# Kernel optimization log

Measured on AMD Instinct MI355X. Metric: run time of the kernel, lower is better.

## Reference

```python
import jax, jax.numpy as jnp
import numpy as np

N = 100000       # nodes
E = 1600000      # edges (before self loops)
F_IN = 128       # input features
H = 4            # heads
C1, C2 = 32, 16  # per-head channels of conv1/conv2


def setup_inputs() -> dict:
    key = jax.random.key(0)
    ks = jax.random.split(key, 12)
    x = jax.random.normal(ks[0], (N, F_IN), jnp.float32)
    edge_index = jax.random.randint(ks[1], (2, E), 0, N, dtype=jnp.int32)
    s1 = 1.0 / np.sqrt(F_IN)
    s2 = 1.0 / np.sqrt(H * C1)
    return {
        "x": x,
        "edge_index": edge_index,
        "W1": jax.random.normal(ks[2], (F_IN, H * C1), jnp.float32) * s1,
        "a_src1": jax.random.normal(ks[3], (1, H, C1), jnp.float32) * s1,
        "a_dst1": jax.random.normal(ks[4], (1, H, C1), jnp.float32) * s1,
        "b1": jnp.zeros((H * C1,), jnp.float32),
        "W2": jax.random.normal(ks[5], (H * C1, H * C2), jnp.float32) * s2,
        "a_src2": jax.random.normal(ks[6], (1, H, C2), jnp.float32) * s2,
        "a_dst2": jax.random.normal(ks[7], (1, H, C2), jnp.float32) * s2,
        "b2": jnp.zeros((H * C2,), jnp.float32),
        "fc_w": jax.random.normal(ks[8], (H * C2, 2), jnp.float32) * (1.0 / np.sqrt(H * C2)),
        "fc_b": jnp.zeros((2,), jnp.float32),
    }


def gat_layer(x, edge_index, W, a_src, a_dst, b, heads, ch):
    """PyG GATConv: concat=True, negative_slope=0.2 (self loops already in edge_index)."""
    n = x.shape[0]
    h = (x @ W).reshape(n, heads, ch)                      # [N,H,C]
    alpha_src = jnp.sum(h * a_src, axis=-1)                # [N,H]
    alpha_dst = jnp.sum(h * a_dst, axis=-1)                # [N,H]
    src, dst = edge_index[0], edge_index[1]                # edge j->i: src=j, dst=i
    e = jax.nn.leaky_relu(alpha_src[src] + alpha_dst[dst], 0.2)  # [E,H]
    # scatter-softmax over incoming edges of each destination node
    m = jax.ops.segment_max(e, dst, num_segments=n)
    m = jnp.where(jnp.isfinite(m), m, 0.0)
    ex = jnp.exp(e - m[dst])
    s = jax.ops.segment_sum(ex, dst, num_segments=n)
    alpha = ex / s[dst]                                    # self loops guarantee s > 0
    out = jax.ops.segment_sum(alpha[:, :, None] * h[src], dst, num_segments=n)
    return out.reshape(n, heads * ch) + b


def reference(x, edge_index, W1, a_src1, a_dst1, b1, W2, a_src2, a_dst2, b2, fc_w, fc_b):
    n = x.shape[0]
    loops = jnp.arange(n, dtype=edge_index.dtype)
    ei = jnp.concatenate([edge_index, jnp.stack([loops, loops])], axis=1)  # add self loops once
    h = jax.nn.relu(gat_layer(x, ei, W1, a_src1, a_dst1, b1, H, C1))
    h = gat_layer(h, ei, W2, a_src2, a_dst2, b2, H, C2)
    g = jnp.sum(h, axis=0, keepdims=True)  # global_add_pool, batch = all zeros -> single graph
    return g @ fc_w + fc_b
```

## Files before the change

kernel.cpp:

```cpp
#include <hip/hip_runtime.h>
#include <hip/hip_bf16.h>
#include <math.h>


using pkh2 = decltype(__builtin_amdgcn_cvt_pkrtz(0.f, 0.f));
typedef __fp16 half8v __attribute__((ext_vector_type(8)));
typedef __attribute__((ext_vector_type(4))) float f32x4;

__device__ __forceinline__ unsigned cvt2h(float a, float b) {
    pkh2 r = __builtin_amdgcn_cvt_pkrtz(a, b);
    return __builtin_bit_cast(unsigned, r);
}
__device__ __forceinline__ unsigned short f2h(float f) {
    return __builtin_bit_cast(unsigned short, (_Float16)f);
}

__device__ __forceinline__ float fdot2b(unsigned wp, unsigned hp, float c) {
#if __has_builtin(__builtin_amdgcn_fdot2)
    return __builtin_amdgcn_fdot2(__builtin_bit_cast(pkh2, wp),
                                  __builtin_bit_cast(pkh2, hp), c, false);
#else
    pkh2 w = __builtin_bit_cast(pkh2, wp), h = __builtin_bit_cast(pkh2, hp);
    return fmaf((float)w[0], (float)h[0], fmaf((float)w[1], (float)h[1], c));
#endif
}


#define BCAP_LOG 13

__global__ __launch_bounds__(256) void bin_scatter_k(const int* __restrict__ ei,
                                                     int* __restrict__ bucketFill,
                                                     int2* __restrict__ binned,
                                                     int E, int N) {
    __shared__ int cnt[512];
    __shared__ int base[512];
    const int ITEMS = E + N;
    const int t = threadIdx.x;
    const int chunk0 = blockIdx.x * 4096;
    for (int b = t; b < 512; b += 256) cnt[b] = 0;
    __syncthreads();
    int s[16], d[16], r[16];
#pragma unroll
    for (int j = 0; j < 16; j++) {
        int i = chunk0 + j * 256 + t;
        if (i < ITEMS) {
            if (i < E) { s[j] = ei[i]; d[j] = ei[E + i]; }
            else       { s[j] = d[j] = i - E; }
            r[j] = atomicAdd(&cnt[d[j] >> 8], 1);
        } else d[j] = -1;
    }
    __syncthreads();
    for (int b = t; b < 512; b += 256) {
        int c = cnt[b];
        base[b] = c ? atomicAdd(&bucketFill[b], c) : 0;
    }
    __syncthreads();
#pragma unroll
    for (int j = 0; j < 16; j++)
        if (d[j] >= 0) {
            int b = d[j] >> 8;
            binned[((size_t)b << BCAP_LOG) + base[b] + r[j]] = make_int2(s[j], d[j]);
        }
}

__global__ void bucket_scan_k(const int* __restrict__ bucketCnt,
                              int* __restrict__ bucketOff, int NB) {
    __shared__ int ls[512];
    int t = threadIdx.x;
    int v = (t < NB) ? bucketCnt[t] : 0;
    ls[t] = v;
    __syncthreads();
    for (int off = 1; off < 512; off <<= 1) {
        int a = (t >= off) ? ls[t - off] : 0;
        __syncthreads();
        ls[t] += a;
        __syncthreads();
    }
    if (t < NB) bucketOff[t] = ls[t] - v;
}

__global__ void csr_build_k(const int2* __restrict__ binned,
                            const int* __restrict__ bucketOff,
                            const int* __restrict__ bucketCnt,
                            int* __restrict__ offs, int* __restrict__ csr,
                            int N, int ITEMS) {
    __shared__ int cnt[256];
    __shared__ int obase[256];
    __shared__ int fill[256];
    const int b = blockIdx.x, t = threadIdx.x;
    cnt[t] = 0; fill[t] = 0;
    __syncthreads();
    const int c = bucketCnt[b];
    const int2* bp = &binned[(size_t)b << BCAP_LOG];
    for (int i = t; i < c; i += 256)
        atomicAdd(&cnt[bp[i].y & 255], 1);
    __syncthreads();
    int v = cnt[t];
    obase[t] = v;
    __syncthreads();
    for (int off = 1; off < 256; off <<= 1) {
        int a = (t >= off) ? obase[t - off] : 0;
        __syncthreads();
        obase[t] += a;
        __syncthreads();
    }
    obase[t] -= v;
    const int beg = bucketOff[b];
    int node = b * 256 + t;
    if (node < N) offs[node] = beg + obase[t];
    if (node == N - 1) offs[N] = ITEMS;
    __syncthreads();
    for (int i = t; i < c; i += 256) {
        int2 sd = bp[i];
        int r = atomicAdd(&fill[sd.y & 255], 1);
        csr[beg + obase[sd.y & 255] + r] = sd.x;
    }
}


template<int NCOL, bool XF16>
__global__ __launch_bounds__(256) void gemm_alpha_mfma(
        const void* __restrict__ Xv, const float* __restrict__ W,
        const float* __restrict__ asrc, const float* __restrict__ adst,
        unsigned short* __restrict__ Y, float* __restrict__ As,
        float* __restrict__ Ad, int M) {
    constexpr int NT = NCOL / 16;
    __shared__ alignas(16) short alds[4 * 4 * 64 * 8];
    __shared__ alignas(16) short blds[NT * 4 * 64 * 8];

    const int t    = threadIdx.x;
    const int w    = t >> 6, lane = t & 63;
    const int row0 = blockIdx.x * 64;

    if constexpr (!XF16) {
        const float* X = (const float*)Xv;
#pragma unroll
        for (int i = 0; i < 8; i++) {
            int flat = (i * 256 + t) * 4;
            int r = flat >> 7, k0 = flat & 127;
            int gr = row0 + r;
            float4 v = make_float4(0.f, 0.f, 0.f, 0.f);
            if (gr < M) v = *(const float4*)&X[(size_t)gr * 128 + k0];
            uint2 u = make_uint2(cvt2h(v.x, v.y), cvt2h(v.z, v.w));
            int frag = ((r >> 4) * 4 + (k0 >> 5)) * 64 + ((((k0 & 31) >> 3) << 4) | (r & 15));
            *(uint2*)&alds[frag * 8 + (k0 & 7)] = u;
        }
    } else {
        const unsigned short* X = (const unsigned short*)Xv;
#pragma unroll
        for (int i = 0; i < 4; i++) {
            int flat = (i * 256 + t) * 8;
            int r = flat >> 7, k0 = flat & 127;
            int gr = row0 + r;
            uint4 v = make_uint4(0u, 0u, 0u, 0u);
            if (gr < M) v = *(const uint4*)&X[(size_t)gr * 128 + k0];
            int frag = ((r >> 4) * 4 + (k0 >> 5)) * 64 + ((((k0 & 31) >> 3) << 4) | (r & 15));
            *(uint4*)&alds[frag * 8] = v;
        }
    }

    {
        constexpr int KQ = 256 / NCOL;
        constexpr int BITER = 32 / KQ;
        int c = t % NCOL, kq = t / NCOL;
        int nt = c >> 4, n = c & 15;
#pragma unroll
        for (int i = 0; i < BITER; i++) {
            int k0 = (i * KQ + kq) * 4;
            uint2 u = make_uint2(
                cvt2h(W[(size_t)(k0 + 0) * NCOL + c], W[(size_t)(k0 + 1) * NCOL + c]),
                cvt2h(W[(size_t)(k0 + 2) * NCOL + c], W[(size_t)(k0 + 3) * NCOL + c]));
            int frag = (nt * 4 + (k0 >> 5)) * 64 + ((((k0 & 31) >> 3) << 4) | n);
            *(uint2*)&blds[frag * 8 + (k0 & 7)] = u;
        }
    }
    __syncthreads();

    f32x4 acc[NT];
#pragma unroll
    for (int nt = 0; nt < NT; nt++) acc[nt] = (f32x4){0.f, 0.f, 0.f, 0.f};
#pragma unroll
    for (int ks = 0; ks < 4; ks++) {
        half8v a = *(half8v*)&alds[((w * 4 + ks) * 64 + lane) * 8];
#pragma unroll
        for (int nt = 0; nt < NT; nt++) {
            half8v b = *(half8v*)&blds[((nt * 4 + ks) * 64 + lane) * 8];
            acc[nt] = __builtin_amdgcn_mfma_f32_16x16x32_f16(a, b, acc[nt], 0, 0, 0);
        }
    }

    const int g = lane >> 4, col = lane & 15;
    float ps[4][4] = {}, pd[4][4] = {};
#pragma unroll
    for (int nt = 0; nt < NT; nt++) {
        float av = asrc[nt * 16 + col];
        float dv = adst[nt * 16 + col];
        int h = (NCOL == 128) ? (nt >> 1) : nt;
#pragma unroll
        for (int j = 0; j < 4; j++) {
            float v = acc[nt][j];
            ps[j][h] = fmaf(v, av, ps[j][h]);
            pd[j][h] = fmaf(v, dv, pd[j][h]);
            int gr = row0 + w * 16 + 4 * g + j;
            if (gr < M) Y[(size_t)gr * NCOL + nt * 16 + col] = f2h(v);
        }
    }
#pragma unroll
    for (int m = 1; m < 16; m <<= 1) {
#pragma unroll
        for (int j = 0; j < 4; j++)
#pragma unroll
            for (int h = 0; h < 4; h++) {
                ps[j][h] += __shfl_xor(ps[j][h], m);
                pd[j][h] += __shfl_xor(pd[j][h], m);
            }
    }
    if (col == 0) {
#pragma unroll
        for (int j = 0; j < 4; j++) {
            int gr = row0 + w * 16 + 4 * g + j;
            if (gr < M) {
#pragma unroll
                for (int h = 0; h < 4; h++) {
                    As[gr * 4 + h] = ps[j][h];
                    Ad[gr * 4 + h] = pd[j][h];
                }
            }
        }
    }
}


template<bool RELU>
__global__ void agg128_k(const unsigned short* __restrict__ Hb,
                         const float* __restrict__ As, const float* __restrict__ Ad,
                         const int* __restrict__ offs, const int* __restrict__ csr,
                         const float* __restrict__ bias,
                         unsigned short* __restrict__ Outb, int n) {
    int wid  = (blockIdx.x * blockDim.x + threadIdx.x) >> 6;
    int lane = threadIdx.x & 63;
    if (wid >= n) return;
    const int g = lane >> 4;
    const int q = lane & 15;
    const int head = q >> 2;
    const int beg = offs[wid], end = offs[wid + 1];
    const float ad = Ad[wid * 4 + head];
    float acc[8];
#pragma unroll
    for (int k = 0; k < 8; k++) acc[k] = 0.f;
    float sw = 0.f;

    for (int cb = beg; cb < end; cb += 64) {
        const int nc = min(64, end - cb);
        const int sreg = csr[cb + (lane < nc ? lane : 0)];
        const int ncr = (nc + 15) & ~15;
        for (int j = 0; j < ncr; j += 16) {
            const int e0 = j + g, e1 = e0 + 4, e2 = e0 + 8, e3 = e0 + 12;
            const bool v0 = e0 < nc, v1 = e1 < nc, v2 = e2 < nc, v3 = e3 < nc;
            const int s0 = __shfl(sreg, v0 ? e0 : 0);
            const int s1 = __shfl(sreg, v1 ? e1 : 0);
            const int s2 = __shfl(sreg, v2 ? e2 : 0);
            const int s3 = __shfl(sreg, v3 ? e3 : 0);
            const uint4 hA = *(const uint4*)&Hb[(size_t)s0 * 128 + q * 8];
            const uint4 hB = *(const uint4*)&Hb[(size_t)s1 * 128 + q * 8];
            const uint4 hC = *(const uint4*)&Hb[(size_t)s2 * 128 + q * 8];
            const uint4 hD = *(const uint4*)&Hb[(size_t)s3 * 128 + q * 8];
            float ev0 = As[s0 * 4 + head] + ad; ev0 = ev0 > 0.f ? ev0 : 0.2f * ev0;
            float ev1 = As[s1 * 4 + head] + ad; ev1 = ev1 > 0.f ? ev1 : 0.2f * ev1;
            float ev2 = As[s2 * 4 + head] + ad; ev2 = ev2 > 0.f ? ev2 : 0.2f * ev2;
            float ev3 = As[s3 * 4 + head] + ad; ev3 = ev3 > 0.f ? ev3 : 0.2f * ev3;
            const float w0 = v0 ? __expf(ev0) : 0.f;
            const float w1 = v1 ? __expf(ev1) : 0.f;
            const float w2 = v2 ? __expf(ev2) : 0.f;
            const float w3 = v3 ? __expf(ev3) : 0.f;
            sw += (w0 + w1) + (w2 + w3);
            const unsigned wp01 = cvt2h(w0, w1);
            const unsigned wp23 = cvt2h(w2, w3);
#pragma unroll
            for (int k = 0; k < 4; k++) {
                unsigned a0 = (&hA.x)[k], a1 = (&hB.x)[k];
                unsigned a2 = (&hC.x)[k], a3 = (&hD.x)[k];
                acc[2 * k]     = fdot2b(wp01, __builtin_amdgcn_perm(a1, a0, 0x05040100u), acc[2 * k]);
                acc[2 * k]     = fdot2b(wp23, __builtin_amdgcn_perm(a3, a2, 0x05040100u), acc[2 * k]);
                acc[2 * k + 1] = fdot2b(wp01, __builtin_amdgcn_perm(a1, a0, 0x07060302u), acc[2 * k + 1]);
                acc[2 * k + 1] = fdot2b(wp23, __builtin_amdgcn_perm(a3, a2, 0x07060302u), acc[2 * k + 1]);
            }
        }
    }

    sw += __shfl_xor(sw, 16); sw += __shfl_xor(sw, 32);
#pragma unroll
    for (int k = 0; k < 8; k++) {
        acc[k] += __shfl_xor(acc[k], 16);
        acc[k] += __shfl_xor(acc[k], 32);
    }
    if (g == 0) {
        const float inv = 1.f / sw;
        float o[8];
#pragma unroll
        for (int k = 0; k < 8; k++) {
            float v = fmaf(acc[k], inv, bias[q * 8 + k]);
            if (RELU) v = fmaxf(v, 0.f);
            o[k] = v;
        }
        uint4 ov = make_uint4(cvt2h(o[0], o[1]), cvt2h(o[2], o[3]),
                              cvt2h(o[4], o[5]), cvt2h(o[6], o[7]));
        *(uint4*)&Outb[(size_t)wid * 128 + q * 8] = ov;
    }
}


__global__ __launch_bounds__(256) void agg64_pool_k(
        const unsigned short* __restrict__ Hb,
        const float* __restrict__ As, const float* __restrict__ Ad,
        const int* __restrict__ offs, const int* __restrict__ csr,
        float* __restrict__ part, int n) {
    __shared__ float gl[64];
    const int t = threadIdx.x;
    if (t < 64) gl[t] = 0.f;
    __syncthreads();
    const int wave0  = (blockIdx.x * blockDim.x + t) >> 6;
    const int nWaves = (gridDim.x * blockDim.x) >> 6;
    const int lane = t & 63;
    const int g = lane >> 3;
    const int q = lane & 7;
    const int head = q >> 1;
    float gsum[8];
#pragma unroll
    for (int k = 0; k < 8; k++) gsum[k] = 0.f;

    for (int wid = wave0; wid < n; wid += nWaves) {
        const int beg = offs[wid], end = offs[wid + 1];
        const float ad = Ad[wid * 4 + head];
        float acc[8];
#pragma unroll
        for (int k = 0; k < 8; k++) acc[k] = 0.f;
        float sw = 0.f;
        for (int cb = beg; cb < end; cb += 64) {
            const int nc = min(64, end - cb);
            const int sreg = csr[cb + (lane < nc ? lane : 0)];
            const int ncr = (nc + 31) & ~31;
            for (int j = 0; j < ncr; j += 32) {
                const int e0 = j + g, e1 = e0 + 8, e2 = e0 + 16, e3 = e0 + 24;
                const bool v0 = e0 < nc, v1 = e1 < nc, v2 = e2 < nc, v3 = e3 < nc;
                const int s0 = __shfl(sreg, v0 ? e0 : 0);
                const int s1 = __shfl(sreg, v1 ? e1 : 0);
                const int s2 = __shfl(sreg, v2 ? e2 : 0);
                const int s3 = __shfl(sreg, v3 ? e3 : 0);
                const uint4 hA = *(const uint4*)&Hb[(size_t)s0 * 64 + q * 8];
                const uint4 hB = *(const uint4*)&Hb[(size_t)s1 * 64 + q * 8];
                const uint4 hC = *(const uint4*)&Hb[(size_t)s2 * 64 + q * 8];
                const uint4 hD = *(const uint4*)&Hb[(size_t)s3 * 64 + q * 8];
                float ev0 = As[s0 * 4 + head] + ad; ev0 = ev0 > 0.f ? ev0 : 0.2f * ev0;
                float ev1 = As[s1 * 4 + head] + ad; ev1 = ev1 > 0.f ? ev1 : 0.2f * ev1;
                float ev2 = As[s2 * 4 + head] + ad; ev2 = ev2 > 0.f ? ev2 : 0.2f * ev2;
                float ev3 = As[s3 * 4 + head] + ad; ev3 = ev3 > 0.f ? ev3 : 0.2f * ev3;
                const float w0 = v0 ? __expf(ev0) : 0.f;
                const float w1 = v1 ? __expf(ev1) : 0.f;
                const float w2 = v2 ? __expf(ev2) : 0.f;
                const float w3 = v3 ? __expf(ev3) : 0.f;
                sw += (w0 + w1) + (w2 + w3);
                const unsigned wp01 = cvt2h(w0, w1);
                const unsigned wp23 = cvt2h(w2, w3);
#pragma unroll
                for (int k = 0; k < 4; k++) {
                    unsigned a0 = (&hA.x)[k], a1 = (&hB.x)[k];
                    unsigned a2 = (&hC.x)[k], a3 = (&hD.x)[k];
                    acc[2 * k]     = fdot2b(wp01, __builtin_amdgcn_perm(a1, a0, 0x05040100u), acc[2 * k]);
                    acc[2 * k]     = fdot2b(wp23, __builtin_amdgcn_perm(a3, a2, 0x05040100u), acc[2 * k]);
                    acc[2 * k + 1] = fdot2b(wp01, __builtin_amdgcn_perm(a1, a0, 0x07060302u), acc[2 * k + 1]);
                    acc[2 * k + 1] = fdot2b(wp23, __builtin_amdgcn_perm(a3, a2, 0x07060302u), acc[2 * k + 1]);
                }
            }
        }
        sw += __shfl_xor(sw, 8); sw += __shfl_xor(sw, 16); sw += __shfl_xor(sw, 32);
#pragma unroll
        for (int k = 0; k < 8; k++) {
            acc[k] += __shfl_xor(acc[k], 8);
            acc[k] += __shfl_xor(acc[k], 16);
            acc[k] += __shfl_xor(acc[k], 32);
        }
        if (g == 0) {
            const float inv = 1.f / sw;
#pragma unroll
            for (int k = 0; k < 8; k++) gsum[k] = fmaf(acc[k], inv, gsum[k]);
        }
    }

    if (g == 0) {
#pragma unroll
        for (int k = 0; k < 8; k++) atomicAdd(&gl[q * 8 + k], gsum[k]);
    }
    __syncthreads();
    if (t < 64) part[(size_t)blockIdx.x * 64 + t] = gl[t];
}


__global__ __launch_bounds__(1024) void reduce_fc_k(
        const float* __restrict__ part, const float* __restrict__ b2,
        const float* __restrict__ w, const float* __restrict__ b,
        float* __restrict__ out, int n, int nPart) {
    __shared__ float ls[1024];
    const int t = threadIdx.x;
    const int c = t & 63, pg = t >> 6;
    float acc = 0.f;
    for (int p = pg; p < nPart; p += 16) acc += part[(size_t)p * 64 + c];
    ls[t] = acc;
    __syncthreads();
    if (t < 64) {
        float s = 0.f;
#pragma unroll
        for (int i = 0; i < 16; i++) s += ls[i * 64 + t];
        ls[t] = s + (float)n * b2[t];
    }
    __syncthreads();
    if (t < 2) {
        float a = b[t];
        for (int cc = 0; cc < 64; cc++) a = fmaf(ls[cc], w[cc * 2 + t], a);
        out[t] = a;
    }
}


static inline size_t align256(size_t x) { return (x + 255) & ~(size_t)255; }

extern "C" void kernel_launch(void* const* d_in, const int* in_sizes, int n_in,
                              void* d_out, int out_size, void* d_ws, size_t ws_size,
                              hipStream_t stream) {
    const float* x     = (const float*)d_in[0];
    const int*   ei    = (const int*)  d_in[1];
    const float* W1    = (const float*)d_in[2];
    const float* asrc1 = (const float*)d_in[3];
    const float* adst1 = (const float*)d_in[4];
    const float* b1    = (const float*)d_in[5];
    const float* W2    = (const float*)d_in[6];
    const float* asrc2 = (const float*)d_in[7];
    const float* adst2 = (const float*)d_in[8];
    const float* b2    = (const float*)d_in[9];
    const float* fcw   = (const float*)d_in[10];
    const float* fcb   = (const float*)d_in[11];
    float* out = (float*)d_out;

    const int N = in_sizes[0] / 128;
    const int E = in_sizes[1] / 2;
    const int ITEMS = E + N;
    const int NB = (N + 255) >> 8;
    const int NPOOL = 2048;

    char* w = (char*)d_ws;
    size_t off = 0;
    int* offs  = (int*)(w + off); off = align256(off + (size_t)(N + 1) * 4);
    int* bOff  = (int*)(w + off); off = align256(off + 512 * 4);
    int* bFill = (int*)(w + off); off = align256(off + 512 * 4);
    int* csr   = (int*)(w + off); off = align256(off + (size_t)ITEMS * 4);
    int2* binned = (int2*)(w + off); off = align256(off + ((size_t)NB << 13) * 8);
    float* As = (float*)(w + off); off = align256(off + (size_t)N * 4 * 4);
    float* Ad = (float*)(w + off); off = align256(off + (size_t)N * 4 * 4);
    float* part = (float*)(w + off); off = align256(off + (size_t)NPOOL * 64 * 4);
    unsigned short* bufH = (unsigned short*)(w + off); off = align256(off + (size_t)N * 128 * 2);
    unsigned short* bufO = (unsigned short*)(w + off); off = align256(off + (size_t)N * 128 * 2);

    hipMemsetAsync(bFill, 0, 512 * sizeof(int), stream);
    bin_scatter_k<<<(ITEMS + 4095) / 4096, 256, 0, stream>>>(ei, bFill, binned, E, N);
    bucket_scan_k<<<1, 512, 0, stream>>>(bFill, bOff, NB);
    csr_build_k<<<NB, 256, 0, stream>>>(binned, bOff, bFill, offs, csr, N, ITEMS);

    gemm_alpha_mfma<128, false><<<(N + 63) / 64, 256, 0, stream>>>(
        x, W1, asrc1, adst1, bufH, As, Ad, N);
    agg128_k<true><<<(N * 64 + 255) / 256, 256, 0, stream>>>(
        bufH, As, Ad, offs, csr, b1, bufO, N);

    gemm_alpha_mfma<64, true><<<(N + 63) / 64, 256, 0, stream>>>(
        bufO, W2, asrc2, adst2, bufH, As, Ad, N);
    agg64_pool_k<<<NPOOL, 256, 0, stream>>>(
        bufH, As, Ad, offs, csr, part, N);

    reduce_fc_k<<<1, 1024, 0, stream>>>(part, b2, fcw, fcb, out, N, NPOOL);
}
```

Before: 248.3 us.

## Pack binned edges into 32-bit words and fold bucket scan into CSR build

Binned edge entries shrink from an int2 pair to one 32-bit word holding the 24-bit source id and the low 8 bits of the destination, halving the traffic of the binning buffer. The separate single-block bucket_scan kernel is removed. Each csr_build block now computes its own bucket offset by summing the preceding bucket counts with a block reduction, which saves a launch and its serialization. This assumes node ids fit in 24 bits and adds redundant prefix-sum work in every block.

```diff
diff --git a/kernel.cpp b/kernel.cpp
--- a/kernel.cpp
+++ b/kernel.cpp
@@ -30,7 +30,7 @@
 
 __global__ __launch_bounds__(256) void bin_scatter_k(const int* __restrict__ ei,
                                                      int* __restrict__ bucketFill,
-                                                     int2* __restrict__ binned,
+                                                     unsigned* __restrict__ binned,
                                                      int E, int N) {
     __shared__ int cnt[512];
     __shared__ int base[512];
@@ -59,41 +59,34 @@
     for (int j = 0; j < 16; j++)
         if (d[j] >= 0) {
             int b = d[j] >> 8;
-            binned[((size_t)b << BCAP_LOG) + base[b] + r[j]] = make_int2(s[j], d[j]);
-        }
-}
-
-__global__ void bucket_scan_k(const int* __restrict__ bucketCnt,
-                              int* __restrict__ bucketOff, int NB) {
-    __shared__ int ls[512];
-    int t = threadIdx.x;
-    int v = (t < NB) ? bucketCnt[t] : 0;
-    ls[t] = v;
-    __syncthreads();
-    for (int off = 1; off < 512; off <<= 1) {
-        int a = (t >= off) ? ls[t - off] : 0;
-        __syncthreads();
-        ls[t] += a;
-        __syncthreads();
-    }
-    if (t < NB) bucketOff[t] = ls[t] - v;
-}
-
-__global__ void csr_build_k(const int2* __restrict__ binned,
-                            const int* __restrict__ bucketOff,
+            binned[((size_t)b << BCAP_LOG) + base[b] + r[j]] =
+                (unsigned)s[j] | ((unsigned)(d[j] & 255) << 24);
+        }
+}
+
+__global__ void csr_build_k(const unsigned* __restrict__ binned,
                             const int* __restrict__ bucketCnt,
                             int* __restrict__ offs, int* __restrict__ csr,
-                            int N, int ITEMS) {
+                            int N, int ITEMS, int NB) {
     __shared__ int cnt[256];
     __shared__ int obase[256];
     __shared__ int fill[256];
+    __shared__ int red[256];
     const int b = blockIdx.x, t = threadIdx.x;
+    int pre = 0;
+    for (int i = t; i < b; i += 256) pre += bucketCnt[i];
+    red[t] = pre;
     cnt[t] = 0; fill[t] = 0;
     __syncthreads();
+    for (int offr = 128; offr >= 1; offr >>= 1) {
+        if (t < offr) red[t] += red[t + offr];
+        __syncthreads();
+    }
+    const int beg = red[0];
     const int c = bucketCnt[b];
-    const int2* bp = &binned[(size_t)b << BCAP_LOG];
+    const unsigned* bp = &binned[(size_t)b << BCAP_LOG];
     for (int i = t; i < c; i += 256)
-        atomicAdd(&cnt[bp[i].y & 255], 1);
+        atomicAdd(&cnt[bp[i] >> 24], 1);
     __syncthreads();
     int v = cnt[t];
     obase[t] = v;
@@ -105,15 +98,15 @@
         __syncthreads();
     }
     obase[t] -= v;
-    const int beg = bucketOff[b];
     int node = b * 256 + t;
     if (node < N) offs[node] = beg + obase[t];
     if (node == N - 1) offs[N] = ITEMS;
     __syncthreads();
     for (int i = t; i < c; i += 256) {
-        int2 sd = bp[i];
-        int r = atomicAdd(&fill[sd.y & 255], 1);
-        csr[beg + obase[sd.y & 255] + r] = sd.x;
+        unsigned p = bp[i];
+        int dlow = p >> 24;
+        int r = atomicAdd(&fill[dlow], 1);
+        csr[beg + obase[dlow] + r] = (int)(p & 0xFFFFFFu);
     }
 }
 
@@ -450,10 +443,9 @@
     char* w = (char*)d_ws;
     size_t off = 0;
     int* offs  = (int*)(w + off); off = align256(off + (size_t)(N + 1) * 4);
-    int* bOff  = (int*)(w + off); off = align256(off + 512 * 4);
     int* bFill = (int*)(w + off); off = align256(off + 512 * 4);
     int* csr   = (int*)(w + off); off = align256(off + (size_t)ITEMS * 4);
-    int2* binned = (int2*)(w + off); off = align256(off + ((size_t)NB << 13) * 8);
+    unsigned* binned = (unsigned*)(w + off); off = align256(off + ((size_t)NB << 13) * 4);
     float* As = (float*)(w + off); off = align256(off + (size_t)N * 4 * 4);
     float* Ad = (float*)(w + off); off = align256(off + (size_t)N * 4 * 4);
     float* part = (float*)(w + off); off = align256(off + (size_t)NPOOL * 64 * 4);
@@ -462,8 +454,7 @@
 
     hipMemsetAsync(bFill, 0, 512 * sizeof(int), stream);
     bin_scatter_k<<<(ITEMS + 4095) / 4096, 256, 0, stream>>>(ei, bFill, binned, E, N);
-    bucket_scan_k<<<1, 512, 0, stream>>>(bFill, bOff, NB);
-    csr_build_k<<<NB, 256, 0, stream>>>(binned, bOff, bFill, offs, csr, N, ITEMS);
+    csr_build_k<<<NB, 256, 0, stream>>>(binned, bFill, offs, csr, N, ITEMS, NB);
 
     gemm_alpha_mfma<128, false><<<(N + 63) / 64, 256, 0, stream>>>(
         x, W1, asrc1, adst1, bufH, As, Ad, N);
```

Result: no change. 245.7 us (-1.1%).
